# Performance work log

Measured on AMD Instinct MI355X. Metric: run time of the kernel, lower is better.

## Reference

```python
import jax, jax.numpy as jnp
import numpy as np

NUM_ITERATIONS = 3


def squash(s):
    # s: [..., out_channels]; norm over last axis (matches torch squash on squeezed tensor)
    norm = jnp.linalg.norm(s, axis=-1, keepdims=True)
    return (norm ** 2 / (1.0 + norm ** 2)) * (s / norm)


def setup_inputs() -> dict:
    key = jax.random.key(0)
    k1, k2 = jax.random.split(key)
    B, R, C, O, I = 256, 192, 96, 16, 20
    x = jax.random.normal(k1, (B, R, I), dtype=jnp.float32)
    W = jax.random.normal(k2, (R, C, O, I), dtype=jnp.float32)
    return {"x": x, "W": W}


def reference(x, W):
    # u_hat[b,r,c,o] = W[r,c,o,i] @ x[b,r,i]  (torch: matmul(W, x[i]) per batch element)
    u_hat = jnp.einsum('rcoi,bri->brco', W, x)  # [B,R,C,O]
    R, C = W.shape[0], W.shape[1]
    b_ij = jnp.zeros((R, C), dtype=x.dtype)  # shared across batch (torch b_ij is [1,R,C,1])
    v_j = None
    for it in range(NUM_ITERATIONS):
        c_ij = jax.nn.softmax(b_ij, axis=0)                 # softmax over routes (dim=1 in torch)
        s_j = jnp.einsum('rc,brco->bco', c_ij, u_hat)        # weighted sum over routes
        v_j = squash(s_j)                                    # [B,C,O]
        if it < NUM_ITERATIONS - 1:
            # agreement: <u_hat, v_j> averaged over batch (torch mean(dim=0))
            a_ij = jnp.einsum('brco,bco->rc', u_hat, v_j) / x.shape[0]
            b_ij = b_ij + a_ij
    return v_j  # [B, num_capsules, out_channels] (torch returns trailing singleton [B,C,O,1])
```

## Files before the change

### kernel.cpp

```cpp
#include <hip/hip_runtime.h>


#define R_ 192
#define C_ 96
#define O_ 16
#define I_ 20
#define B_ 256
#define K1 3840
#define N_ 1536
#define ZSPLIT 15
#define KCH 256
#define STILE 393216

typedef unsigned short u16;
typedef __attribute__((ext_vector_type(8))) short short8;
typedef __attribute__((ext_vector_type(4))) float floatx4;

__device__ inline float bf2f(u16 h) {
  union { unsigned int u; float f; } x; x.u = ((unsigned int)h) << 16; return x.f;
}
__device__ inline u16 f2bf(float f) {
  union { float f; unsigned int u; } x; x.f = f;
  unsigned int r = x.u + 0x7FFFu + ((x.u >> 16) & 1u);
  return (u16)(r >> 16);
}
__device__ inline unsigned int pack2(float a, float b) {
  return (unsigned int)f2bf(a) | ((unsigned int)f2bf(b) << 16);
}
__device__ inline void async16(const u16* g, u16* l) {
  __builtin_amdgcn_global_load_lds(
      (__attribute__((address_space(1))) void*)(unsigned long long)g,
      (__attribute__((address_space(3))) void*)(unsigned int)(unsigned long long)l,
      16, 0, 0);
}

__global__ void k_prep(const float* __restrict__ W, const float* __restrict__ X,
                       u16* __restrict__ WtT, u16* __restrict__ Xk,
                       u16* __restrict__ xT, float* __restrict__ bij) {
  int bid = blockIdx.x;
  if (bid < 5760) {
    int t = (bid * 256 + threadIdx.x) << 2;
    int n = t / K1, k = t - n * K1;
    int c = n >> 4, o = n & 15;
    const float* Wn = W + (size_t)(c * O_ + o) * I_;
    u16 h[4];
    #pragma unroll
    for (int e = 0; e < 4; ++e) {
      int ke = k + e, r = ke / I_, i = ke - r * I_;
      h[e] = f2bf(Wn[(size_t)r * (C_ * O_ * I_) + i]);
    }
    ushort4 o4; o4.x = h[0]; o4.y = h[1]; o4.z = h[2]; o4.w = h[3];
    *(ushort4*)&WtT[t] = o4;
  } else if (bid < 6000) {
    __shared__ u16 tile[64][72];
    int idx = bid - 5760;
    int kb = (idx % 60) << 6, bb = (idx / 60) << 6;
    int brow = threadIdx.x >> 4;
    int kq = (threadIdx.x & 15) << 2;
    #pragma unroll
    for (int p = 0; p < 4; ++p) {
      int bl = p * 16 + brow;
      float4 v = *(const float4*)(X + (size_t)(bb + bl) * K1 + kb + kq);
      ushort4 h;
      h.x = f2bf(v.x); h.y = f2bf(v.y); h.z = f2bf(v.z); h.w = f2bf(v.w);
      *(ushort4*)(Xk + (size_t)(bb + bl) * K1 + kb + kq) = h;
      tile[kq + 0][bl] = h.x;
      tile[kq + 1][bl] = h.y;
      tile[kq + 2][bl] = h.z;
      tile[kq + 3][bl] = h.w;
    }
    __syncthreads();
    int kr = threadIdx.x >> 3;
    int bq = (threadIdx.x & 7) << 3;
    #pragma unroll
    for (int q = 0; q < 2; ++q) {
      int kl = q * 32 + kr;
      *(uint4*)(xT + (size_t)(kb + kl) * B_ + bb + bq) = *(const uint4*)&tile[kl][bq];
    }
  } else {
    int t = ((bid - 6000) * 256 + threadIdx.x) << 2;
    if (t < R_ * C_) *(float4*)&bij[t] = (float4){0.f, 0.f, 0.f, 0.f};
  }
}

__device__ inline uint4 scale_b8(uint4 raw, int kg, const float* smrow) {
  int r0 = kg / I_;
  int bnd = (r0 + 1) * I_ - kg;
  float s0 = smrow[r0];
  float s1 = smrow[(r0 + 1 < R_) ? r0 + 1 : R_ - 1];
  union { uint4 q; u16 h[8]; } u; u.q = raw;
  #pragma unroll
  for (int j = 0; j < 8; ++j)
    u.h[j] = f2bf(bf2f(u.h[j]) * ((j < bnd) ? s0 : s1));
  return u.q;
}


__global__ __launch_bounds__(256) void gemm1(
    const u16* __restrict__ A, const u16* __restrict__ Bt,
    const float* __restrict__ bij, u16* __restrict__ P, int doScale) {
  __shared__ u16 As[2][8192];
  __shared__ u16 Bs[2][4096];
  __shared__ float sm[4][192];
  int tid = threadIdx.x;
  int w = tid >> 6, lane = tid & 63;
  if (doScale) {
    int c = (blockIdx.y << 2) + w;
    float e0 = bij[c * R_ + lane];
    float e1 = bij[c * R_ + lane + 64];
    float e2 = bij[c * R_ + lane + 128];
    float mx = fmaxf(e0, fmaxf(e1, e2));
    #pragma unroll
    for (int off = 32; off > 0; off >>= 1) mx = fmaxf(mx, __shfl_xor(mx, off));
    e0 = expf(e0 - mx); e1 = expf(e1 - mx); e2 = expf(e2 - mx);
    float s = e0 + e1 + e2;
    #pragma unroll
    for (int off = 32; off > 0; off >>= 1) s += __shfl_xor(s, off);
    float inv = 1.0f / s;
    sm[w][lane] = e0 * inv;
    sm[w][lane + 64] = e1 * inv;
    sm[w][lane + 128] = e2 * inv;
  }

  long m0 = (long)blockIdx.x * 128, n0 = (long)blockIdx.y * 64;
  int k0 = blockIdx.z * KCH;
  const u16* Ab = A + m0 * K1 + k0;
  const u16* Bb = Bt + n0 * K1 + k0;
  int q_s = ((lane & 3) - ((lane >> 3) & 3)) & 3;
  const u16* AgC[4]; int AlC[4];
  #pragma unroll
  for (int m = 0; m < 4; ++m) {
    AgC[m] = Ab + (long)(((m & 1) << 6) + (w << 4) + (lane >> 2)) * K1
             + ((m >> 1) << 5) + (q_s << 3);
    AlC[m] = (m << 11) + (w << 9);
  }
  const u16* BgC[2]; int BlC[2];
  #pragma unroll
  for (int m = 0; m < 2; ++m) {
    BgC[m] = Bb + (long)((w << 4) + (lane >> 2)) * K1 + (m << 5) + (q_s << 3);
    BlC[m] = (m << 11) + (w << 9);
  }
  int rowD = tid >> 2;
  int qD = ((tid & 3) - ((tid >> 3) & 3)) & 3;
  const u16* Bgs = Bb + (long)rowD * K1 + (qD << 3);
  const float* smrow = &sm[w][0];
  int wm = (w >> 1) << 6, wn = (w & 1) << 5;
  int quad = lane >> 4, lrow = lane & 15;
  int swz = ((quad + (lrow >> 1)) & 3) << 3;
  floatx4 acc[4][2];
  #pragma unroll
  for (int a = 0; a < 4; ++a)
    #pragma unroll
    for (int b = 0; b < 2; ++b) acc[a][b] = (floatx4){0.f, 0.f, 0.f, 0.f};

  #pragma unroll
  for (int m = 0; m < 4; ++m) async16(AgC[m], &As[0][AlC[m]]);
  uint4 b0, b1;
  if (doScale) {
    b0 = *(const uint4*)Bgs;
    b1 = *(const uint4*)(Bgs + 32);
  } else {
    async16(BgC[0], &Bs[0][BlC[0]]);
    async16(BgC[1], &Bs[0][BlC[1]]);
  }
  __syncthreads();

  int p = 0;
  for (int kt = 0; kt < 4; ++kt) {
    if (doScale) {
      int kg = k0 + (kt << 6) + (qD << 3);
      *(uint4*)&Bs[p][tid << 3] = scale_b8(b0, kg, smrow);
      *(uint4*)&Bs[p][2048 + (tid << 3)] = scale_b8(b1, kg + 32, smrow);
      __syncthreads();
    } else if (kt > 0) {
      __syncthreads();
    }
    if (kt + 1 < 4) {
      int kk = (kt + 1) << 6;
      #pragma unroll
      for (int m = 0; m < 4; ++m) async16(AgC[m] + kk, &As[p ^ 1][AlC[m]]);
      if (doScale) {
        b0 = *(const uint4*)(Bgs + kk);
        b1 = *(const uint4*)(Bgs + kk + 32);
      } else {
        async16(BgC[0] + kk, &Bs[p ^ 1][BlC[0]]);
        async16(BgC[1] + kk, &Bs[p ^ 1][BlC[1]]);
      }
    }
    #pragma unroll
    for (int s = 0; s < 2; ++s) {
      short8 af[4], bfr[2];
      #pragma unroll
      for (int ms = 0; ms < 4; ++ms)
        af[ms] = *(const short8*)&As[p][(s << 12)
                                        + ((wm + ms * 16 + lrow) << 5) + swz];
      #pragma unroll
      for (int ns = 0; ns < 2; ++ns)
        bfr[ns] = *(const short8*)&Bs[p][(s << 11)
                                         + ((wn + ns * 16 + lrow) << 5) + swz];
      #pragma unroll
      for (int ms = 0; ms < 4; ++ms)
        #pragma unroll
        for (int ns = 0; ns < 2; ++ns)
          acc[ms][ns] = __builtin_amdgcn_mfma_f32_16x16x32_bf16(
              af[ms], bfr[ns], acc[ms][ns], 0, 0, 0);
    }
    p ^= 1;
  }
  size_t zb = (size_t)blockIdx.z * (size_t)STILE;
  #pragma unroll
  for (int ms = 0; ms < 4; ++ms)
    #pragma unroll
    for (int ns = 0; ns < 2; ++ns) {
      int b = (int)m0 + wm + ms * 16 + (quad << 2);
      int n = (int)n0 + wn + ns * 16 + lrow;
      uint2 pk;
      pk.x = pack2(acc[ms][ns][0], acc[ms][ns][1]);
      pk.y = pack2(acc[ms][ns][2], acc[ms][ns][3]);
      *(uint2*)&P[zb + (size_t)n * B_ + b] = pk;
    }
}

__global__ void k_redsq(const u16* __restrict__ P, float* __restrict__ out,
                        u16* __restrict__ vT, float preScale, int last) {
  __shared__ float nsq_l[4][64];
  int c = blockIdx.x, bh = blockIdx.y;
  int lane = threadIdx.x & 63, og = threadIdx.x >> 6;
  int b = (bh << 6) + lane;
  int n0 = (c << 4) + (og << 2);
  float acc[4];
  #pragma unroll
  for (int oo = 0; oo < 4; ++oo) acc[oo] = 0.f;
  #pragma unroll
  for (int z = 0; z < ZSPLIT; ++z) {
    size_t base = (size_t)z * STILE + (size_t)n0 * B_ + b;
    #pragma unroll
    for (int oo = 0; oo < 4; ++oo)
      acc[oo] += bf2f(P[base + (size_t)oo * B_]);
  }
  #pragma unroll
  for (int oo = 0; oo < 4; ++oo) acc[oo] *= preScale;
  float q = acc[0] * acc[0] + acc[1] * acc[1] + acc[2] * acc[2] + acc[3] * acc[3];
  nsq_l[og][lane] = q;
  __syncthreads();
  float nsq = nsq_l[0][lane] + nsq_l[1][lane] + nsq_l[2][lane] + nsq_l[3][lane];
  float f = nsq / ((1.0f + nsq) * sqrtf(nsq));
  #pragma unroll
  for (int oo = 0; oo < 4; ++oo) acc[oo] *= f;
  if (last) {
    *(float4*)(out + (size_t)b * N_ + n0) = (float4){acc[0], acc[1], acc[2], acc[3]};
  } else {
    #pragma unroll
    for (int oo = 0; oo < 4; ++oo)
      vT[(size_t)(n0 + oo) * B_ + b] = f2bf(acc[oo]);
  }
}

__global__ __launch_bounds__(256) void gemm2_agree(
    const u16* __restrict__ A, const u16* __restrict__ Bt,
    const u16* __restrict__ WtT, float* __restrict__ bij) {
  const int K = 256;
  __shared__ u16 As[2][8192];
  __shared__ u16 Bs[2][4096];
  int tid = threadIdx.x;
  long m0 = (long)blockIdx.x * 128, n0 = (long)blockIdx.y * 64;
  const u16* Ab = A + m0 * K;
  const u16* Bb = Bt + n0 * K;
  int w = tid >> 6, lane = tid & 63;
  int wm = (w >> 1) << 6, wn = (w & 1) << 5;
  int quad = lane >> 4, lrow = lane & 15;
  int swz = ((quad + (lrow >> 1)) & 3) << 3;
  int q_s = ((lane & 3) - ((lane >> 3) & 3)) & 3;
  const u16* AgC[4]; int AlC[4];
  #pragma unroll
  for (int m = 0; m < 4; ++m) {
    AgC[m] = Ab + (long)(((m & 1) << 6) + (w << 4) + (lane >> 2)) * K
             + ((m >> 1) << 5) + (q_s << 3);
    AlC[m] = (m << 11) + (w << 9);
  }
  const u16* BgC[2]; int BlC[2];
  #pragma unroll
  for (int m = 0; m < 2; ++m) {
    BgC[m] = Bb + (long)((w << 4) + (lane >> 2)) * K + (m << 5) + (q_s << 3);
    BlC[m] = (m << 11) + (w << 9);
  }
  floatx4 acc[4][2];
  #pragma unroll
  for (int a = 0; a < 4; ++a)
    #pragma unroll
    for (int b = 0; b < 2; ++b) acc[a][b] = (floatx4){0.f, 0.f, 0.f, 0.f};

  #pragma unroll
  for (int m = 0; m < 4; ++m) async16(AgC[m], &As[0][AlC[m]]);
  async16(BgC[0], &Bs[0][BlC[0]]);
  async16(BgC[1], &Bs[0][BlC[1]]);

  int p = 0;
  #pragma unroll
  for (int kt = 0; kt < 4; ++kt) {
    __syncthreads();
    if (kt + 1 < 4) {
      int kk = (kt + 1) << 6;
      #pragma unroll
      for (int m = 0; m < 4; ++m) async16(AgC[m] + kk, &As[p ^ 1][AlC[m]]);
      async16(BgC[0] + kk, &Bs[p ^ 1][BlC[0]]);
      async16(BgC[1] + kk, &Bs[p ^ 1][BlC[1]]);
    }
    #pragma unroll
    for (int s = 0; s < 2; ++s) {
      short8 af[4], bfr[2];
      #pragma unroll
      for (int ms = 0; ms < 4; ++ms)
        af[ms] = *(const short8*)&As[p][(s << 12)
                                        + ((wm + ms * 16 + lrow) << 5) + swz];
      #pragma unroll
      for (int ns = 0; ns < 2; ++ns)
        bfr[ns] = *(const short8*)&Bs[p][(s << 11)
                                         + ((wn + ns * 16 + lrow) << 5) + swz];
      #pragma unroll
      for (int ms = 0; ms < 4; ++ms)
        #pragma unroll
        for (int ns = 0; ns < 2; ++ns)
          acc[ms][ns] = __builtin_amdgcn_mfma_f32_16x16x32_bf16(
              af[ms], bfr[ns], acc[ms][ns], 0, 0, 0);
    }
    p ^= 1;
  }
  #pragma unroll
  for (int ms = 0; ms < 4; ++ms) {
    int rowbase = (int)m0 + wm + ms * 16;
    int r_lo = rowbase / I_;
    int r_hi = (rowbase + 15) / I_;
    int bnd = (r_lo + 1) * I_;
    int rowl = rowbase + (quad << 2);
    #pragma unroll
    for (int ns = 0; ns < 2; ++ns) {
      int col = (int)n0 + wn + ns * 16 + lrow;
      uint2 wv = *(const uint2*)&WtT[(size_t)col * K1 + rowl];
      u16 h[4];
      h[0] = (u16)(wv.x & 0xffff); h[1] = (u16)(wv.x >> 16);
      h[2] = (u16)(wv.y & 0xffff); h[3] = (u16)(wv.y >> 16);
      float p0 = 0.f, p1 = 0.f;
      #pragma unroll
      for (int e = 0; e < 4; ++e) {
        float pr = acc[ms][ns][e] * bf2f(h[e]);
        if (rowl + e < bnd) p0 += pr; else p1 += pr;
      }
      #pragma unroll
      for (int off = 32; off > 0; off >>= 1) {
        p0 += __shfl_xor(p0, off);
        p1 += __shfl_xor(p1, off);
      }
      if (lane == 0) {
        int c = col >> 4;
        atomicAdd(&bij[c * R_ + r_lo], p0 * (1.0f / 256.0f));
        atomicAdd(&bij[c * R_ + r_hi], p1 * (1.0f / 256.0f));
      }
    }
  }
}

extern "C" void kernel_launch(void* const* d_in, const int* in_sizes, int n_in,
                              void* d_out, int out_size, void* d_ws, size_t ws_size,
                              hipStream_t stream) {
  const float* X = (const float*)d_in[0];
  const float* W = (const float*)d_in[1];
  float* out = (float*)d_out;
  char* ws = (char*)d_ws;
  u16*  WtT = (u16*)(ws);
  u16*  Xk  = (u16*)(ws + 11796480);
  u16*  xT  = (u16*)(ws + 13762560);
  u16*  vT  = (u16*)(ws + 15728640);
  u16*  Pb  = (u16*)(ws + 16515072);
  float* bij = (float*)(ws + 28311552);

  k_prep<<<6018, 256, 0, stream>>>(W, X, WtT, Xk, xT, bij);

  for (int it = 0; it < 3; ++it) {
    gemm1<<<dim3(2, 24, ZSPLIT), 256, 0, stream>>>(Xk, WtT, bij, Pb, it > 0);
    k_redsq<<<dim3(96, 4), 256, 0, stream>>>(
        Pb, out, vT, it == 0 ? (1.0f / 192.0f) : 1.0f, it == 2);
    if (it < 2)
      gemm2_agree<<<dim3(30, 24), 256, 0, stream>>>(xT, vT, WtT, bij);
  }
}
```

Baseline: 149.1 us.

## Vectorize split-K reduction loads and stage W tile through LDS in agreement GEMM

k_redsq now reads 8 bf16 partials per thread with 128-bit loads, stages the sums in shared memory, computes the squash factor per batch row, and writes out and vT with wide stores. The grid is halved to 96x2 blocks, each covering 128 batch rows. gemm2_agree prefetches its W tile into registers with coalesced 128-bit loads before the main loop, then transposes it into reused LDS for the epilogue. This replaces the scattered 8-byte global gathers in the epilogue and the 2-byte strided loads in the reduction, at the cost of extra LDS traffic, two barriers and more register pressure.

```diff
diff --git a/kernel.cpp b/kernel.cpp
--- a/kernel.cpp
+++ b/kernel.cpp
@@ -223,36 +223,53 @@
 
 __global__ void k_redsq(const u16* __restrict__ P, float* __restrict__ out,
                         u16* __restrict__ vT, float preScale, int last) {
-  __shared__ float nsq_l[4][64];
+  __shared__ float sv[16][128];
+  __shared__ float f_l[128];
   int c = blockIdx.x, bh = blockIdx.y;
-  int lane = threadIdx.x & 63, og = threadIdx.x >> 6;
-  int b = (bh << 6) + lane;
-  int n0 = (c << 4) + (og << 2);
-  float acc[4];
-  #pragma unroll
-  for (int oo = 0; oo < 4; ++oo) acc[oo] = 0.f;
+  int t = threadIdx.x;
+  int n = t >> 4, bg = t & 15;
+  const u16* base = P + (size_t)((c << 4) + n) * B_ + (bh << 7) + (bg << 3);
+  float a[8];
+  #pragma unroll
+  for (int j = 0; j < 8; ++j) a[j] = 0.f;
   #pragma unroll
   for (int z = 0; z < ZSPLIT; ++z) {
-    size_t base = (size_t)z * STILE + (size_t)n0 * B_ + b;
-    #pragma unroll
-    for (int oo = 0; oo < 4; ++oo)
-      acc[oo] += bf2f(P[base + (size_t)oo * B_]);
-  }
-  #pragma unroll
-  for (int oo = 0; oo < 4; ++oo) acc[oo] *= preScale;
-  float q = acc[0] * acc[0] + acc[1] * acc[1] + acc[2] * acc[2] + acc[3] * acc[3];
-  nsq_l[og][lane] = q;
+    union { uint4 q; u16 h[8]; } u;
+    u.q = *(const uint4*)(base + (size_t)z * STILE);
+    #pragma unroll
+    for (int j = 0; j < 8; ++j) a[j] += bf2f(u.h[j]);
+  }
+  #pragma unroll
+  for (int j = 0; j < 8; ++j) sv[n][(bg << 3) + j] = a[j] * preScale;
   __syncthreads();
-  float nsq = nsq_l[0][lane] + nsq_l[1][lane] + nsq_l[2][lane] + nsq_l[3][lane];
-  float f = nsq / ((1.0f + nsq) * sqrtf(nsq));
-  #pragma unroll
-  for (int oo = 0; oo < 4; ++oo) acc[oo] *= f;
+  if (t < 128) {
+    float nsq = 0.f;
+    #pragma unroll
+    for (int o = 0; o < 16; ++o) { float v = sv[o][t]; nsq += v * v; }
+    f_l[t] = nsq / ((1.0f + nsq) * sqrtf(nsq));
+  }
+  __syncthreads();
   if (last) {
-    *(float4*)(out + (size_t)b * N_ + n0) = (float4){acc[0], acc[1], acc[2], acc[3]};
+    int bl = t >> 1, oh = (t & 1) << 3;
+    float fv = f_l[bl];
+    float* op = out + (size_t)((bh << 7) + bl) * N_ + (c << 4) + oh;
+    float4 v0, v1;
+    v0.x = sv[oh + 0][bl] * fv; v0.y = sv[oh + 1][bl] * fv;
+    v0.z = sv[oh + 2][bl] * fv; v0.w = sv[oh + 3][bl] * fv;
+    v1.x = sv[oh + 4][bl] * fv; v1.y = sv[oh + 5][bl] * fv;
+    v1.z = sv[oh + 6][bl] * fv; v1.w = sv[oh + 7][bl] * fv;
+    *(float4*)op = v0;
+    *(float4*)(op + 4) = v1;
   } else {
-    #pragma unroll
-    for (int oo = 0; oo < 4; ++oo)
-      vT[(size_t)(n0 + oo) * B_ + b] = f2bf(acc[oo]);
+    int bs = bg << 3;
+    uint4 o4; unsigned int* po = (unsigned int*)&o4;
+    #pragma unroll
+    for (int j = 0; j < 4; ++j) {
+      float lo = sv[n][bs + 2 * j]     * f_l[bs + 2 * j];
+      float hi = sv[n][bs + 2 * j + 1] * f_l[bs + 2 * j + 1];
+      po[j] = pack2(lo, hi);
+    }
+    *(uint4*)&vT[(size_t)((c << 4) + n) * B_ + (bh << 7) + bs] = o4;
   }
 }
 
@@ -271,6 +288,15 @@
   int quad = lane >> 4, lrow = lane & 15;
   int swz = ((quad + (lrow >> 1)) & 3) << 3;
   int q_s = ((lane & 3) - ((lane >> 3) & 3)) & 3;
+
+  uint4 wreg[4];
+  #pragma unroll
+  for (int j = 0; j < 4; ++j) {
+    int idx = (j << 8) + tid;
+    wreg[j] = *(const uint4*)&WtT[(size_t)(n0 + (idx >> 4)) * K1 + m0
+                                  + ((idx & 15) << 3)];
+  }
+
   const u16* AgC[4]; int AlC[4];
   #pragma unroll
   for (int m = 0; m < 4; ++m) {
@@ -326,17 +352,29 @@
     }
     p ^= 1;
   }
+
+  __syncthreads();
+  u16* Ws = (u16*)As;
+  #pragma unroll
+  for (int j = 0; j < 4; ++j) {
+    int idx = (j << 8) + tid;
+    *(uint4*)&Ws[(((idx & 15) << 6) + (idx >> 4)) << 3] = wreg[j];
+  }
+  __syncthreads();
+
   #pragma unroll
   for (int ms = 0; ms < 4; ++ms) {
     int rowbase = (int)m0 + wm + ms * 16;
     int r_lo = rowbase / I_;
     int r_hi = (rowbase + 15) / I_;
     int bnd = (r_lo + 1) * I_;
-    int rowl = rowbase + (quad << 2);
+    int rlL = wm + ms * 16 + (quad << 2);
+    int rowl = (int)m0 + rlL;
+    int wbase = ((rlL >> 3) << 9) + ((rlL & 4) ? 4 : 0);
     #pragma unroll
     for (int ns = 0; ns < 2; ++ns) {
-      int col = (int)n0 + wn + ns * 16 + lrow;
-      uint2 wv = *(const uint2*)&WtT[(size_t)col * K1 + rowl];
+      int colL = wn + ns * 16 + lrow;
+      uint2 wv = *(const uint2*)&Ws[wbase + (colL << 3)];
       u16 h[4];
       h[0] = (u16)(wv.x & 0xffff); h[1] = (u16)(wv.x >> 16);
       h[2] = (u16)(wv.y & 0xffff); h[3] = (u16)(wv.y >> 16);
@@ -352,7 +390,7 @@
         p1 += __shfl_xor(p1, off);
       }
       if (lane == 0) {
-        int c = col >> 4;
+        int c = ((int)n0 + colL) >> 4;
         atomicAdd(&bij[c * R_ + r_lo], p0 * (1.0f / 256.0f));
         atomicAdd(&bij[c * R_ + r_hi], p1 * (1.0f / 256.0f));
       }
@@ -378,7 +416,7 @@
 
   for (int it = 0; it < 3; ++it) {
     gemm1<<<dim3(2, 24, ZSPLIT), 256, 0, stream>>>(Xk, WtT, bij, Pb, it > 0);
-    k_redsq<<<dim3(96, 4), 256, 0, stream>>>(
+    k_redsq<<<dim3(96, 2), 256, 0, stream>>>(
         Pb, out, vT, it == 0 ? (1.0f / 192.0f) : 1.0f, it == 2);
     if (it < 2)
       gemm2_agree<<<dim3(30, 24), 256, 0, stream>>>(xT, vT, WtT, bij);
```

After: 158.5 us. 6.3% more time.
